# Kernel tuning notes

Hardware: AMD Instinct MI355X
Metric: run time of the kernel (lower is better)

## Reference

```python
import jax, jax.numpy as jnp
import numpy as np

EMBED_DIM = 512
NUM_HEADS = 8
HEAD_DIM = EMBED_DIM // NUM_HEADS


def setup_inputs() -> dict:
    key = jax.random.key(0)
    k_x, k_qkv, k_proj, k_pb = jax.random.split(key, 4)
    B, N, C = 2, 4096, EMBED_DIM
    x = jax.random.normal(k_x, (B, N, C), dtype=jnp.float32)
    # nn.Linear(embed_dim, 3*embed_dim, bias=False): weight [3C, C], y = x @ W.T
    s = 1.0 / np.sqrt(C)
    w_qkv = jax.random.uniform(k_qkv, (3 * C, C), dtype=jnp.float32, minval=-s, maxval=s)
    w_proj = jax.random.uniform(k_proj, (C, C), dtype=jnp.float32, minval=-s, maxval=s)
    b_proj = jax.random.uniform(k_pb, (C,), dtype=jnp.float32, minval=-s, maxval=s)
    return {"x": x, "w_qkv": w_qkv, "w_proj": w_proj, "b_proj": b_proj}


def reference(x, w_qkv, w_proj, b_proj):
    B, N, C = x.shape
    H, D = NUM_HEADS, HEAD_DIM
    scale = D ** -0.5
    qkv = jnp.einsum('bnc,fc->bnf', x, w_qkv)           # [B, N, 3C]
    qkv = qkv.reshape(B, N, 3, H, D)
    q, k, v = [jnp.transpose(qkv[:, :, i], (0, 2, 1, 3)) for i in range(3)]  # [B,H,N,D]
    attn = jnp.einsum('bhnd,bhmd->bhnm', q, k) * scale  # [B,H,N,N]
    # additive causal mask: -inf above the diagonal
    causal = jnp.triu(jnp.full((N, N), -jnp.inf, dtype=attn.dtype), k=1)
    attn = jax.nn.softmax(attn + causal, axis=-1)
    out = jnp.einsum('bhnm,bhmd->bhnd', attn, v)        # [B,H,N,D]
    out = jnp.transpose(out, (0, 2, 1, 3)).reshape(B, N, C)
    return jnp.einsum('bnc,oc->bno', out, w_proj) + b_proj
```

## Files before the change

kernel.cpp:

```cpp
#include <hip/hip_runtime.h>
#include <hip/hip_bf16.h>


typedef __attribute__((ext_vector_type(8))) short s16x8;
typedef __attribute__((ext_vector_type(4))) float f32x4;

#define QSCALE 0.18033688011112042f

__device__ __forceinline__ ushort f2bf(float f) {
  unsigned u = __float_as_uint(f);
  u = (u + 0x7FFFu + ((u >> 16) & 1u)) >> 16;
  return (ushort)u;
}

__device__ __forceinline__ unsigned cvt_pk_bf16(float a, float b) {
  unsigned r;
  asm("v_cvt_pk_bf16_f32 %0, %1, %2" : "=v"(r) : "v"(a), "v"(b));
  return r;
}

__device__ __forceinline__ float bflo(unsigned u) { return __uint_as_float(u << 16); }
__device__ __forceinline__ float bfhi(unsigned u) { return __uint_as_float(u & 0xffff0000u); }

__global__ __launch_bounds__(256) void cvt_all(const float* __restrict__ x,
                                               const float* __restrict__ wq,
                                               const float* __restrict__ wp,
                                               ushort* __restrict__ xb,
                                               ushort* __restrict__ wqb,
                                               ushort* __restrict__ wpb) {
  int i = blockIdx.x * 256 + threadIdx.x;
  const float* src;
  ushort* dst;
  int off;
  if (i < 1048576) {
    src = x; dst = xb; off = i;
  } else if (i < 1245184) {
    src = wq; dst = wqb; off = i - 1048576;
  } else {
    src = wp; dst = wpb; off = i - 1245184;
  }
  float4 v = reinterpret_cast<const float4*>(src)[off];
  ushort4 o;
  o.x = f2bf(v.x); o.y = f2bf(v.y); o.z = f2bf(v.z); o.w = f2bf(v.w);
  reinterpret_cast<ushort4*>(dst)[off] = o;
}

template <int EPI>
__global__ __launch_bounds__(256) void gemm_bt(const ushort* __restrict__ A,
                                               const ushort* __restrict__ W,
                                               ushort* __restrict__ q_ws,
                                               ushort* __restrict__ k_ws,
                                               ushort* __restrict__ vt_ws,
                                               float* __restrict__ outf,
                                               const float* __restrict__ bias) {
  __shared__ ushort As[2][128 * 32];
  __shared__ ushort Bs[2][128 * 32];
  const int tid = threadIdx.x;
  const int lane = tid & 63, wv = tid >> 6;
  const int wm = wv >> 1, wn = wv & 1;
  const int l15 = lane & 15, g = lane >> 4;
  const int tm = blockIdx.y * 128, tn = blockIdx.x * 128;

  f32x4 acc[4][4] = {};

#define GSTAGE(BUF, K0)                                                                    \
  do {                                                                                     \
    _Pragma("unroll") for (int it = 0; it < 2; ++it) {                                     \
      int slot = it * 256 + tid;                                                           \
      int row = slot >> 2;                                                                 \
      int ch = (slot & 3) ^ ((row >> 1) & 3);                                              \
      const int sb = (it * 256 + wv * 64) * 8;        \
      __builtin_amdgcn_global_load_lds(                                                    \
          (const __attribute__((address_space(1))) void*)(A + (size_t)(tm + row) * 512 +   \
                                                          (K0) + ch * 8),                  \
          (__attribute__((address_space(3))) void*)(&As[BUF][0] + sb), 16, 0, 0);          \
      __builtin_amdgcn_global_load_lds(                                                    \
          (const __attribute__((address_space(1))) void*)(W + (size_t)(tn + row) * 512 +   \
                                                          (K0) + ch * 8),                  \
          (__attribute__((address_space(3))) void*)(&Bs[BUF][0] + sb), 16, 0, 0);          \
    }                                                                                      \
  } while (0)

  GSTAGE(0, 0);
  __syncthreads();
  int cur = 0;
  for (int t = 0; t < 16; ++t) {
    if (t < 15) GSTAGE(cur ^ 1, (t + 1) * 32);
    s16x8 af[4], bfr[4];
#pragma unroll
    for (int i = 0; i < 4; ++i) {
      int Ra = wm * 64 + i * 16 + l15;
      af[i] = reinterpret_cast<const s16x8*>(&As[cur][0])[Ra * 4 + (g ^ ((Ra >> 1) & 3))];
      int Rb = wn * 64 + i * 16 + l15;
      bfr[i] = reinterpret_cast<const s16x8*>(&Bs[cur][0])[Rb * 4 + (g ^ ((Rb >> 1) & 3))];
    }
#pragma unroll
    for (int mi = 0; mi < 4; ++mi)
#pragma unroll
      for (int ni = 0; ni < 4; ++ni)
        acc[mi][ni] =
            __builtin_amdgcn_mfma_f32_16x16x32_bf16(af[mi], bfr[ni], acc[mi][ni], 0, 0, 0);
    __syncthreads();
    cur ^= 1;
  }
#undef GSTAGE

  const int rowb = tm + wm * 64 + g * 4;
  const int colb = tn + wn * 64 + l15;
#pragma unroll
  for (int mi = 0; mi < 4; ++mi) {
#pragma unroll
    for (int ni = 0; ni < 4; ++ni) {
      int r0 = rowb + mi * 16;
      int col = colb + ni * 16;
      if (EPI == 0) {
        int i3 = col >> 9, h = (col >> 6) & 7, d = col & 63;
        int b = r0 >> 12;
        int bh = b * 8 + h;
        if (i3 == 2) {
          int n0 = r0 & 4095;
          int kt = n0 >> 6, ce = (n0 >> 5) & 1, ge = (n0 >> 3) & 3, je = n0 & 7;
          int nbe = d >> 4, le = d & 15;
          ushort4 pk;
          pk.x = f2bf(acc[mi][ni][0]);
          pk.y = f2bf(acc[mi][ni][1]);
          pk.z = f2bf(acc[mi][ni][2]);
          pk.w = f2bf(acc[mi][ni][3]);
          *reinterpret_cast<ushort4*>(
              vt_ws + (((size_t)bh * 64 + kt) * 8 + nbe * 2 + ce) * 512 + (ge * 16 + le) * 8 +
              je) = pk;
        } else if (i3 == 1) {
          int ce = d >> 5, ge = (d >> 3) & 3, je = d & 7;
#pragma unroll
          for (int r = 0; r < 4; ++r) {
            int n = (r0 + r) & 4095;
            int kt = n >> 6, le = n & 15, nbe = (n >> 4) & 3;
            k_ws[(((size_t)bh * 64 + kt) * 8 + nbe * 2 + ce) * 512 + (ge * 16 + le) * 8 + je] =
                f2bf(acc[mi][ni][r]);
          }
        } else {
          int n0 = r0 & 4095;
#pragma unroll
          for (int r = 0; r < 4; ++r)
            q_ws[((size_t)bh * 4096 + (n0 + r)) * 64 + d] = f2bf(acc[mi][ni][r] * QSCALE);
        }
      } else {
#pragma unroll
        for (int r = 0; r < 4; ++r)
          outf[(size_t)(r0 + r) * 512 + col] = acc[mi][ni][r] + bias[col];
      }
    }
  }
}

__global__ __launch_bounds__(256, 3) void attn_kernel(const ushort* __restrict__ Q,
                                                      const ushort* __restrict__ Kk,
                                                      const ushort* __restrict__ Vt,
                                                      ushort* __restrict__ po,
                                                      float* __restrict__ ml) {
  __shared__ ushort Ks[2][4096];
  __shared__ ushort Vs[2][4096];
  __shared__ ushort P_lds[4][32 * 64];
  const int tid = threadIdx.x;
  const int lane = tid & 63, wv = tid >> 6;
  const int l15 = lane & 15, g = lane >> 4;
  const int L = blockIdx.x;
  const int p = L & 7;
  int j2 = L >> 3;
  {
    const int pos = j2 & 31, quarter = j2 >> 5;
    if (quarter & 1) j2 = quarter * 32 + (31 - pos);
  }
  const int bh = p * 2 + (j2 & 1);
  const int i = j2 >> 1;
  const int G = 31 - (i >> 1);
  const int h = i & 1;
  const int qt = 4 * G + wv;
  const int ktmax = qt >> 1;
  const int mid = G + 1;
  const int klo = h ? mid : 0;
  const int khi = h ? ktmax : (mid - 1);
  const int KLO = h ? mid : 0;
  const int KHI = h ? (2 * G + 1) : (mid - 1);
  const int slot = (bh * 128 + qt) * 2 + h;
  const int qw = qt * 32;
  const size_t baseQ = (size_t)bh * 4096 * 64;

  s16x8 aq[2][2];
#pragma unroll
  for (int s = 0; s < 2; ++s) {
    const ushort* qp = Q + baseQ + (size_t)(qw + s * 16 + l15) * 64 + g * 8;
    aq[s][0] = *reinterpret_cast<const s16x8*>(qp);
    aq[s][1] = *reinterpret_cast<const s16x8*>(qp + 32);
  }

  f32x4 o[2][4] = {};
  float m[2] = {-1e30f, -1e30f};
  float l[2] = {0.f, 0.f};
  const int swz = (l15 & 7) << 3;
  ushort* pl = P_lds[wv];

#define KVSTAGE(BUF, KT)                                                                  \
  do {                                                                                    \
    const ushort* kSrc = Kk + ((size_t)bh * 64 + (KT)) * 4096;                            \
    const ushort* vSrc = Vt + ((size_t)bh * 64 + (KT)) * 4096;                            \
    _Pragma("unroll") for (int c = 0; c < 2; ++c) {                                       \
      const int sb = (c * 256 + wv * 64) * 8;        \
      __builtin_amdgcn_global_load_lds(                                                   \
          (const __attribute__((address_space(1))) void*)(kSrc + sb + lane * 8),          \
          (__attribute__((address_space(3))) void*)(&Ks[BUF][0] + sb), 16, 0, 0);         \
      __builtin_amdgcn_global_load_lds(                                                   \
          (const __attribute__((address_space(1))) void*)(vSrc + sb + lane * 8),          \
          (__attribute__((address_space(3))) void*)(&Vs[BUF][0] + sb), 16, 0, 0);         \
    }                                                                                     \
  } while (0)

  KVSTAGE(0, KLO);
  __syncthreads();
  int cur = 0;
  for (int kt = KLO; kt <= KHI; ++kt) {
    if (kt < KHI) KVSTAGE(cur ^ 1, kt + 1);
    if (kt >= klo && kt <= khi) {
      const ushort* kl = &Ks[cur][lane * 8];
      const ushort* vl = &Vs[cur][lane * 8];
      s16x8 kf[8], vf[8];
#pragma unroll
      for (int t = 0; t < 8; ++t) kf[t] = *reinterpret_cast<const s16x8*>(kl + t * 512);
#pragma unroll
      for (int t = 0; t < 8; ++t) vf[t] = *reinterpret_cast<const s16x8*>(vl + t * 512);
      f32x4 st[2][4] = {};
      __builtin_amdgcn_s_setprio(1);
#pragma unroll
      for (int nb = 0; nb < 4; ++nb)
#pragma unroll
        for (int s = 0; s < 2; ++s) {
          st[s][nb] = __builtin_amdgcn_mfma_f32_16x16x32_bf16(kf[nb * 2 + 0], aq[s][0],
                                                              st[s][nb], 0, 0, 0);
          st[s][nb] = __builtin_amdgcn_mfma_f32_16x16x32_bf16(kf[nb * 2 + 1], aq[s][1],
                                                              st[s][nb], 0, 0, 0);
        }
      __builtin_amdgcn_s_setprio(0);
      if (kt == ktmax) {
        const int k0d = kt * 64;
#pragma unroll
        for (int s = 0; s < 2; ++s)
#pragma unroll
          for (int nb = 0; nb < 4; ++nb)
#pragma unroll
            for (int r2 = 0; r2 < 4; ++r2)
              if (k0d + nb * 16 + g * 4 + r2 > qw + s * 16 + l15) st[s][nb][r2] = -1e30f;
      }
#pragma unroll
      for (int s = 0; s < 2; ++s) {
        float a0 = fmaxf(fmaxf(st[s][0][0], st[s][0][1]), fmaxf(st[s][0][2], st[s][0][3]));
        float a1 = fmaxf(fmaxf(st[s][1][0], st[s][1][1]), fmaxf(st[s][1][2], st[s][1][3]));
        float a2 = fmaxf(fmaxf(st[s][2][0], st[s][2][1]), fmaxf(st[s][2][2], st[s][2][3]));
        float a3 = fmaxf(fmaxf(st[s][3][0], st[s][3][1]), fmaxf(st[s][3][2], st[s][3][3]));
        float pm = fmaxf(fmaxf(a0, a1), fmaxf(a2, a3));
        if (!__all(pm - m[s] <= 8.0f)) {
          float pmf = fmaxf(pm, __shfl_xor(pm, 16));
          pmf = fmaxf(pmf, __shfl_xor(pmf, 32));
          const float mn = fmaxf(m[s], pmf);
          const float al = __builtin_amdgcn_exp2f(m[s] - mn);
          l[s] *= al;
          m[s] = mn;
#pragma unroll
          for (int nb = 0; nb < 4; ++nb)
#pragma unroll
            for (int r2 = 0; r2 < 4; ++r2) o[s][nb][r2] *= al;
        }
        float rs = 0.f;
#pragma unroll
        for (int nb = 0; nb < 4; ++nb) {
          float p0 = __builtin_amdgcn_exp2f(st[s][nb][0] - m[s]);
          float p1 = __builtin_amdgcn_exp2f(st[s][nb][1] - m[s]);
          float p2 = __builtin_amdgcn_exp2f(st[s][nb][2] - m[s]);
          float p3 = __builtin_amdgcn_exp2f(st[s][nb][3] - m[s]);
          rs += (p0 + p1) + (p2 + p3);
          uint2 w;
          w.x = cvt_pk_bf16(p0, p1);
          w.y = cvt_pk_bf16(p2, p3);
          *reinterpret_cast<uint2*>(pl + (s * 16 + l15) * 64 + ((nb * 16 + g * 4) ^ swz)) = w;
        }
        l[s] += rs;
      }
      s16x8 pa[2][2];
#pragma unroll
      for (int s = 0; s < 2; ++s)
#pragma unroll
        for (int c = 0; c < 2; ++c)
          pa[s][c] = *reinterpret_cast<const s16x8*>(pl + (s * 16 + l15) * 64 +
                                                     ((c * 32 + g * 8) ^ swz));
      __builtin_amdgcn_s_setprio(1);
#pragma unroll
      for (int nb = 0; nb < 4; ++nb)
#pragma unroll
        for (int s = 0; s < 2; ++s) {
          o[s][nb] = __builtin_amdgcn_mfma_f32_16x16x32_bf16(vf[nb * 2 + 0], pa[s][0],
                                                             o[s][nb], 0, 0, 0);
          o[s][nb] = __builtin_amdgcn_mfma_f32_16x16x32_bf16(vf[nb * 2 + 1], pa[s][1],
                                                             o[s][nb], 0, 0, 0);
        }
      __builtin_amdgcn_s_setprio(0);
    }
    __syncthreads();
    cur ^= 1;
  }
#undef KVSTAGE

  float lr[2];
#pragma unroll
  for (int s = 0; s < 2; ++s) {
    float ls = l[s];
    ls += __shfl_xor(ls, 16);
    ls += __shfl_xor(ls, 32);
    lr[s] = ls;
  }

#pragma unroll
  for (int s = 0; s < 2; ++s) {
    const float linv = (lr[s] > 0.f) ? (1.0f / lr[s]) : 0.f;
    const int row = s * 16 + l15;
    const size_t pbase = ((size_t)slot * 32 + row) * 64;
#pragma unroll
    for (int nb = 0; nb < 4; ++nb) {
      uint2 pk;
      pk.x = cvt_pk_bf16(o[s][nb][0] * linv, o[s][nb][1] * linv);
      pk.y = cvt_pk_bf16(o[s][nb][2] * linv, o[s][nb][3] * linv);
      *reinterpret_cast<uint2*>(po + pbase + nb * 16 + g * 4) = pk;
    }
    if (g == 0) {
      float2 v;
      v.x = m[s];
      v.y = lr[s];
      *reinterpret_cast<float2*>(ml + ((size_t)slot * 32 + row) * 2) = v;
    }
  }
}

__global__ __launch_bounds__(64) void attn_merge(const ushort* __restrict__ po,
                                                 const float* __restrict__ ml,
                                                 ushort* __restrict__ O) {
  const int M = blockIdx.x, tid = threadIdx.x;
  const int p = M & 7, q2 = M >> 3;
  const int bh = p * 2 + (q2 & 1);
  const int qt = q2 >> 1;
  const int t = bh * 128 + qt;
  const int row = tid >> 1, dh = (tid & 1) * 32;
  const float2 ml0 = *reinterpret_cast<const float2*>(ml + ((size_t)(t * 2 + 0) * 32 + row) * 2);
  const float2 ml1 = *reinterpret_cast<const float2*>(ml + ((size_t)(t * 2 + 1) * 32 + row) * 2);
  const float ms = fmaxf(ml0.x, ml1.x);
  const float w0 = __builtin_amdgcn_exp2f(ml0.x - ms) * ml0.y;
  const float w1 = __builtin_amdgcn_exp2f(ml1.x - ms) * ml1.y;
  const float inv = 1.0f / (w0 + w1);
  const float c0 = w0 * inv, c1 = w1 * inv;
  const int b = bh >> 3, h = bh & 7;
  const size_t rowo = (size_t)(b * 4096 + qt * 32 + row) * 512 + h * 64 + dh;
  const ushort* p0 = po + ((size_t)(t * 2 + 0) * 32 + row) * 64 + dh;
  const ushort* p1 = po + ((size_t)(t * 2 + 1) * 32 + row) * 64 + dh;
#pragma unroll
  for (int j = 0; j < 4; ++j) {
    uint4 a = reinterpret_cast<const uint4*>(p0)[j];
    uint4 bb = reinterpret_cast<const uint4*>(p1)[j];
    uint4 out;
    out.x = cvt_pk_bf16(c0 * bflo(a.x) + c1 * bflo(bb.x), c0 * bfhi(a.x) + c1 * bfhi(bb.x));
    out.y = cvt_pk_bf16(c0 * bflo(a.y) + c1 * bflo(bb.y), c0 * bfhi(a.y) + c1 * bfhi(bb.y));
    out.z = cvt_pk_bf16(c0 * bflo(a.z) + c1 * bflo(bb.z), c0 * bfhi(a.z) + c1 * bfhi(bb.z));
    out.w = cvt_pk_bf16(c0 * bflo(a.w) + c1 * bflo(bb.w), c0 * bfhi(a.w) + c1 * bfhi(bb.w));
    reinterpret_cast<uint4*>(&O[rowo])[j] = out;
  }
}

extern "C" void kernel_launch(void* const* d_in, const int* in_sizes, int n_in,
                              void* d_out, int out_size, void* d_ws, size_t ws_size,
                              hipStream_t stream) {
  const float* x = (const float*)d_in[0];
  const float* w_qkv = (const float*)d_in[1];
  const float* w_proj = (const float*)d_in[2];
  const float* b_proj = (const float*)d_in[3];
  float* out = (float*)d_out;

  ushort* xb = (ushort*)d_ws;
  ushort* wqkvb = xb + (size_t)8192 * 512;
  ushort* wprojb = wqkvb + (size_t)1536 * 512;
  ushort* qws = wprojb + (size_t)512 * 512;
  ushort* kws = qws + (size_t)16 * 4096 * 64;
  ushort* vtws = kws + (size_t)16 * 4096 * 64;
  ushort* ows = vtws + (size_t)16 * 4096 * 64;

  cvt_all<<<5120, 256, 0, stream>>>(x, w_qkv, w_proj, xb, wqkvb, wprojb);

  gemm_bt<0><<<dim3(12, 64), 256, 0, stream>>>(xb, wqkvb, qws, kws, vtws, nullptr, nullptr);

  ushort* po = ows + (size_t)8192 * 512;
  float* ml = (float*)(po + (size_t)2048 * 2 * 32 * 64);

  attn_kernel<<<1024, 256, 0, stream>>>(qws, kws, vtws, po, ml);
  attn_merge<<<2048, 64, 0, stream>>>(po, ml, ows);

  gemm_bt<1><<<dim3(4, 64), 256, 0, stream>>>(ows, wprojb, nullptr, nullptr, nullptr, out,
                                              b_proj);
}
```

Before: 109.1 us.

## Switch attention to 32x32x16 MFMA with in-register P via permlane32 swap

Rewrites the attention inner loop to use 32x32x16 bf16 MFMA instead of 16x16x32. The Q, K and V^T workspace layouts written by the QKV GEMM epilogue are changed to match the new operand fragments. The softmax probabilities are repacked into B-operand registers with v_permlane32_swap, which removes the per-wave P LDS round trip and its extra reads and writes. Row statistics now need only a single cross-half shuffle. Occupancy hint drops from 3 to 2 blocks per CU because of larger accumulator register use, and V loads are deferred until after the softmax.

```diff
diff --git a/kernel.cpp b/kernel.cpp
--- a/kernel.cpp
+++ b/kernel.cpp
@@ -4,6 +4,8 @@
 
 typedef __attribute__((ext_vector_type(8))) short s16x8;
 typedef __attribute__((ext_vector_type(4))) float f32x4;
+typedef __attribute__((ext_vector_type(16))) float f32x16;
+typedef __attribute__((ext_vector_type(4))) unsigned u32x4;
 
 #define QSCALE 0.18033688011112042f
 
@@ -119,30 +121,35 @@
         int bh = b * 8 + h;
         if (i3 == 2) {
           int n0 = r0 & 4095;
-          int kt = n0 >> 6, ce = (n0 >> 5) & 1, ge = (n0 >> 3) & 3, je = n0 & 7;
-          int nbe = d >> 4, le = d & 15;
+          int kt64 = n0 >> 6, key64 = n0 & 63;
+          int kc = key64 >> 4, hk = (key64 >> 3) & 1, j0 = key64 & 7;
+          int db = d >> 5, d31 = d & 31;
           ushort4 pk;
           pk.x = f2bf(acc[mi][ni][0]);
           pk.y = f2bf(acc[mi][ni][1]);
           pk.z = f2bf(acc[mi][ni][2]);
           pk.w = f2bf(acc[mi][ni][3]);
-          *reinterpret_cast<ushort4*>(
-              vt_ws + (((size_t)bh * 64 + kt) * 8 + nbe * 2 + ce) * 512 + (ge * 16 + le) * 8 +
-              je) = pk;
+          *reinterpret_cast<ushort4*>(vt_ws + (size_t)(bh * 64 + kt64) * 4096 +
+                                      ((db * 4 + kc) * 64 + d31 + 32 * hk) * 8 + j0) = pk;
         } else if (i3 == 1) {
-          int ce = d >> 5, ge = (d >> 3) & 3, je = d & 7;
+          int dt = d >> 4, hd = (d >> 3) & 1, j = d & 7;
 #pragma unroll
           for (int r = 0; r < 4; ++r) {
             int n = (r0 + r) & 4095;
-            int kt = n >> 6, le = n & 15, nbe = (n >> 4) & 3;
-            k_ws[(((size_t)bh * 64 + kt) * 8 + nbe * 2 + ce) * 512 + (ge * 16 + le) * 8 + je] =
-                f2bf(acc[mi][ni][r]);
+            int kt64 = n >> 6, key64 = n & 63;
+            int kb = key64 >> 5, key31 = key64 & 31;
+            k_ws[(size_t)(bh * 64 + kt64) * 4096 +
+                 ((kb * 4 + dt) * 64 + key31 + 32 * hd) * 8 + j] = f2bf(acc[mi][ni][r]);
           }
         } else {
-          int n0 = r0 & 4095;
-#pragma unroll
-          for (int r = 0; r < 4; ++r)
-            q_ws[((size_t)bh * 4096 + (n0 + r)) * 64 + d] = f2bf(acc[mi][ni][r] * QSCALE);
+          int dt = d >> 4, hd = (d >> 3) & 1, j = d & 7;
+#pragma unroll
+          for (int r = 0; r < 4; ++r) {
+            int n = (r0 + r) & 4095;
+            int qt = n >> 5, q31 = n & 31;
+            q_ws[(size_t)(bh * 128 + qt) * 2048 + (dt * 64 + q31 + 32 * hd) * 8 + j] =
+                f2bf(acc[mi][ni][r] * QSCALE);
+          }
         }
       } else {
 #pragma unroll
@@ -153,17 +160,16 @@
   }
 }
 
-__global__ __launch_bounds__(256, 3) void attn_kernel(const ushort* __restrict__ Q,
+__global__ __launch_bounds__(256, 2) void attn_kernel(const ushort* __restrict__ Q,
                                                       const ushort* __restrict__ Kk,
                                                       const ushort* __restrict__ Vt,
                                                       ushort* __restrict__ po,
                                                       float* __restrict__ ml) {
   __shared__ ushort Ks[2][4096];
   __shared__ ushort Vs[2][4096];
-  __shared__ ushort P_lds[4][32 * 64];
   const int tid = threadIdx.x;
   const int lane = tid & 63, wv = tid >> 6;
-  const int l15 = lane & 15, g = lane >> 4;
+  const int l31 = lane & 31, hf = lane >> 5;
   const int L = blockIdx.x;
   const int p = L & 7;
   int j2 = L >> 3;
@@ -184,28 +190,24 @@
   const int KHI = h ? (2 * G + 1) : (mid - 1);
   const int slot = (bh * 128 + qt) * 2 + h;
   const int qw = qt * 32;
-  const size_t baseQ = (size_t)bh * 4096 * 64;
-
-  s16x8 aq[2][2];
-#pragma unroll
-  for (int s = 0; s < 2; ++s) {
-    const ushort* qp = Q + baseQ + (size_t)(qw + s * 16 + l15) * 64 + g * 8;
-    aq[s][0] = *reinterpret_cast<const s16x8*>(qp);
-    aq[s][1] = *reinterpret_cast<const s16x8*>(qp + 32);
-  }
-
-  f32x4 o[2][4] = {};
-  float m[2] = {-1e30f, -1e30f};
-  float l[2] = {0.f, 0.f};
-  const int swz = (l15 & 7) << 3;
-  ushort* pl = P_lds[wv];
+
+  s16x8 aq[4];
+  {
+    const ushort* qp = Q + ((size_t)bh * 128 + qt) * 2048 + lane * 8;
+#pragma unroll
+    for (int dt = 0; dt < 4; ++dt) aq[dt] = *reinterpret_cast<const s16x8*>(qp + dt * 512);
+  }
+
+  f32x16 o[2] = {};
+  float m = -1e30f;
+  float l = 0.f;
 
 #define KVSTAGE(BUF, KT)                                                                  \
   do {                                                                                    \
     const ushort* kSrc = Kk + ((size_t)bh * 64 + (KT)) * 4096;                            \
     const ushort* vSrc = Vt + ((size_t)bh * 64 + (KT)) * 4096;                            \
     _Pragma("unroll") for (int c = 0; c < 2; ++c) {                                       \
-      const int sb = (c * 256 + wv * 64) * 8;        \
+      const int sb = (c * 256 + wv * 64) * 8;                                             \
       __builtin_amdgcn_global_load_lds(                                                   \
           (const __attribute__((address_space(1))) void*)(kSrc + sb + lane * 8),          \
           (__attribute__((address_space(3))) void*)(&Ks[BUF][0] + sb), 16, 0, 0);         \
@@ -222,85 +224,85 @@
     if (kt < KHI) KVSTAGE(cur ^ 1, kt + 1);
     if (kt >= klo && kt <= khi) {
       const ushort* kl = &Ks[cur][lane * 8];
-      const ushort* vl = &Vs[cur][lane * 8];
-      s16x8 kf[8], vf[8];
+      s16x8 kf[8];
 #pragma unroll
       for (int t = 0; t < 8; ++t) kf[t] = *reinterpret_cast<const s16x8*>(kl + t * 512);
-#pragma unroll
-      for (int t = 0; t < 8; ++t) vf[t] = *reinterpret_cast<const s16x8*>(vl + t * 512);
-      f32x4 st[2][4] = {};
+      f32x16 st[2] = {};
       __builtin_amdgcn_s_setprio(1);
 #pragma unroll
-      for (int nb = 0; nb < 4; ++nb)
-#pragma unroll
-        for (int s = 0; s < 2; ++s) {
-          st[s][nb] = __builtin_amdgcn_mfma_f32_16x16x32_bf16(kf[nb * 2 + 0], aq[s][0],
-                                                              st[s][nb], 0, 0, 0);
-          st[s][nb] = __builtin_amdgcn_mfma_f32_16x16x32_bf16(kf[nb * 2 + 1], aq[s][1],
-                                                              st[s][nb], 0, 0, 0);
-        }
+      for (int kb = 0; kb < 2; ++kb)
+#pragma unroll
+        for (int dt = 0; dt < 4; ++dt)
+          st[kb] = __builtin_amdgcn_mfma_f32_32x32x16_bf16(kf[kb * 4 + dt], aq[dt],
+                                                           st[kb], 0, 0, 0);
       __builtin_amdgcn_s_setprio(0);
       if (kt == ktmax) {
-        const int k0d = kt * 64;
-#pragma unroll
-        for (int s = 0; s < 2; ++s)
-#pragma unroll
-          for (int nb = 0; nb < 4; ++nb)
-#pragma unroll
-            for (int r2 = 0; r2 < 4; ++r2)
-              if (k0d + nb * 16 + g * 4 + r2 > qw + s * 16 + l15) st[s][nb][r2] = -1e30f;
-      }
-#pragma unroll
-      for (int s = 0; s < 2; ++s) {
-        float a0 = fmaxf(fmaxf(st[s][0][0], st[s][0][1]), fmaxf(st[s][0][2], st[s][0][3]));
-        float a1 = fmaxf(fmaxf(st[s][1][0], st[s][1][1]), fmaxf(st[s][1][2], st[s][1][3]));
-        float a2 = fmaxf(fmaxf(st[s][2][0], st[s][2][1]), fmaxf(st[s][2][2], st[s][2][3]));
-        float a3 = fmaxf(fmaxf(st[s][3][0], st[s][3][1]), fmaxf(st[s][3][2], st[s][3][3]));
-        float pm = fmaxf(fmaxf(a0, a1), fmaxf(a2, a3));
-        if (!__all(pm - m[s] <= 8.0f)) {
-          float pmf = fmaxf(pm, __shfl_xor(pm, 16));
-          pmf = fmaxf(pmf, __shfl_xor(pmf, 32));
-          const float mn = fmaxf(m[s], pmf);
-          const float al = __builtin_amdgcn_exp2f(m[s] - mn);
-          l[s] *= al;
-          m[s] = mn;
-#pragma unroll
-          for (int nb = 0; nb < 4; ++nb)
-#pragma unroll
-            for (int r2 = 0; r2 < 4; ++r2) o[s][nb][r2] *= al;
+        const int qg = qw + l31;
+#pragma unroll
+        for (int kb = 0; kb < 2; ++kb)
+#pragma unroll
+          for (int r = 0; r < 16; ++r)
+            if (kt * 64 + kb * 32 + (r & 3) + 8 * (r >> 2) + 4 * hf > qg)
+              st[kb][r] = -1e30f;
+      }
+      float mx[2];
+#pragma unroll
+      for (int kb = 0; kb < 2; ++kb) {
+        float t0 = fmaxf(fmaxf(st[kb][0], st[kb][1]), fmaxf(st[kb][2], st[kb][3]));
+        float t1 = fmaxf(fmaxf(st[kb][4], st[kb][5]), fmaxf(st[kb][6], st[kb][7]));
+        float t2 = fmaxf(fmaxf(st[kb][8], st[kb][9]), fmaxf(st[kb][10], st[kb][11]));
+        float t3 = fmaxf(fmaxf(st[kb][12], st[kb][13]), fmaxf(st[kb][14], st[kb][15]));
+        mx[kb] = fmaxf(fmaxf(t0, t1), fmaxf(t2, t3));
+      }
+      float pm = fmaxf(mx[0], mx[1]);
+      if (!__all(pm - m <= 8.0f)) {
+        float pmf = fmaxf(pm, __shfl_xor(pm, 32));
+        const float mn = fmaxf(m, pmf);
+        const float al = __builtin_amdgcn_exp2f(m - mn);
+        l *= al;
+        m = mn;
+#pragma unroll
+        for (int db = 0; db < 2; ++db)
+#pragma unroll
+          for (int r = 0; r < 16; ++r) o[db][r] *= al;
+      }
+      s16x8 pb[4];
+      float rs = 0.f;
+#pragma unroll
+      for (int kb = 0; kb < 2; ++kb) {
+        float e[16];
+#pragma unroll
+        for (int r = 0; r < 16; ++r) {
+          e[r] = __builtin_amdgcn_exp2f(st[kb][r] - m);
+          rs += e[r];
         }
-        float rs = 0.f;
-#pragma unroll
-        for (int nb = 0; nb < 4; ++nb) {
-          float p0 = __builtin_amdgcn_exp2f(st[s][nb][0] - m[s]);
-          float p1 = __builtin_amdgcn_exp2f(st[s][nb][1] - m[s]);
-          float p2 = __builtin_amdgcn_exp2f(st[s][nb][2] - m[s]);
-          float p3 = __builtin_amdgcn_exp2f(st[s][nb][3] - m[s]);
-          rs += (p0 + p1) + (p2 + p3);
-          uint2 w;
-          w.x = cvt_pk_bf16(p0, p1);
-          w.y = cvt_pk_bf16(p2, p3);
-          *reinterpret_cast<uint2*>(pl + (s * 16 + l15) * 64 + ((nb * 16 + g * 4) ^ swz)) = w;
-        }
-        l[s] += rs;
-      }
-      s16x8 pa[2][2];
-#pragma unroll
-      for (int s = 0; s < 2; ++s)
-#pragma unroll
-        for (int c = 0; c < 2; ++c)
-          pa[s][c] = *reinterpret_cast<const s16x8*>(pl + (s * 16 + l15) * 64 +
-                                                     ((c * 32 + g * 8) ^ swz));
+        unsigned a0 = cvt_pk_bf16(e[0], e[1]), a1 = cvt_pk_bf16(e[2], e[3]);
+        unsigned b0 = cvt_pk_bf16(e[4], e[5]), b1 = cvt_pk_bf16(e[6], e[7]);
+        asm volatile("v_permlane32_swap_b32 %0, %1" : "+v"(a0), "+v"(b0));
+        asm volatile("v_permlane32_swap_b32 %0, %1" : "+v"(a1), "+v"(b1));
+        u32x4 w0;
+        w0[0] = a0; w0[1] = a1; w0[2] = b0; w0[3] = b1;
+        pb[kb * 2] = __builtin_bit_cast(s16x8, w0);
+        unsigned c0 = cvt_pk_bf16(e[8], e[9]), c1 = cvt_pk_bf16(e[10], e[11]);
+        unsigned d0 = cvt_pk_bf16(e[12], e[13]), d1 = cvt_pk_bf16(e[14], e[15]);
+        asm volatile("v_permlane32_swap_b32 %0, %1" : "+v"(c0), "+v"(d0));
+        asm volatile("v_permlane32_swap_b32 %0, %1" : "+v"(c1), "+v"(d1));
+        u32x4 w1;
+        w1[0] = c0; w1[1] = c1; w1[2] = d0; w1[3] = d1;
+        pb[kb * 2 + 1] = __builtin_bit_cast(s16x8, w1);
+      }
+      l += rs;
+      const ushort* vl = &Vs[cur][lane * 8];
+      s16x8 vf[8];
+#pragma unroll
+      for (int t = 0; t < 8; ++t) vf[t] = *reinterpret_cast<const s16x8*>(vl + t * 512);
       __builtin_amdgcn_s_setprio(1);
 #pragma unroll
-      for (int nb = 0; nb < 4; ++nb)
-#pragma unroll
-        for (int s = 0; s < 2; ++s) {
-          o[s][nb] = __builtin_amdgcn_mfma_f32_16x16x32_bf16(vf[nb * 2 + 0], pa[s][0],
-                                                             o[s][nb], 0, 0, 0);
-          o[s][nb] = __builtin_amdgcn_mfma_f32_16x16x32_bf16(vf[nb * 2 + 1], pa[s][1],
-                                                             o[s][nb], 0, 0, 0);
-        }
+      for (int db = 0; db < 2; ++db)
+#pragma unroll
+        for (int kc = 0; kc < 4; ++kc)
+          o[db] = __builtin_amdgcn_mfma_f32_32x32x16_bf16(vf[db * 4 + kc], pb[kc],
+                                                          o[db], 0, 0, 0);
       __builtin_amdgcn_s_setprio(0);
     }
     __syncthreads();
@@ -308,33 +310,25 @@
   }
 #undef KVSTAGE
 
-  float lr[2];
-#pragma unroll
-  for (int s = 0; s < 2; ++s) {
-    float ls = l[s];
-    ls += __shfl_xor(ls, 16);
-    ls += __shfl_xor(ls, 32);
-    lr[s] = ls;
-  }
-
-#pragma unroll
-  for (int s = 0; s < 2; ++s) {
-    const float linv = (lr[s] > 0.f) ? (1.0f / lr[s]) : 0.f;
-    const int row = s * 16 + l15;
-    const size_t pbase = ((size_t)slot * 32 + row) * 64;
-#pragma unroll
-    for (int nb = 0; nb < 4; ++nb) {
+  float lr = l + __shfl_xor(l, 32);
+  const float linv = (lr > 0.f) ? (1.0f / lr) : 0.f;
+
+  const size_t pbase = ((size_t)slot * 32 + l31) * 64;
+#pragma unroll
+  for (int db = 0; db < 2; ++db)
+#pragma unroll
+    for (int rg = 0; rg < 4; ++rg) {
+      const int d0 = db * 32 + 8 * rg + 4 * hf;
       uint2 pk;
-      pk.x = cvt_pk_bf16(o[s][nb][0] * linv, o[s][nb][1] * linv);
-      pk.y = cvt_pk_bf16(o[s][nb][2] * linv, o[s][nb][3] * linv);
-      *reinterpret_cast<uint2*>(po + pbase + nb * 16 + g * 4) = pk;
+      pk.x = cvt_pk_bf16(o[db][rg * 4 + 0] * linv, o[db][rg * 4 + 1] * linv);
+      pk.y = cvt_pk_bf16(o[db][rg * 4 + 2] * linv, o[db][rg * 4 + 3] * linv);
+      *reinterpret_cast<uint2*>(po + pbase + d0) = pk;
     }
-    if (g == 0) {
-      float2 v;
-      v.x = m[s];
-      v.y = lr[s];
-      *reinterpret_cast<float2*>(ml + ((size_t)slot * 32 + row) * 2) = v;
-    }
+  if (hf == 0) {
+    float2 v;
+    v.x = m;
+    v.y = lr;
+    *reinterpret_cast<float2*>(ml + ((size_t)slot * 32 + l31) * 2) = v;
   }
 }
 
```

Result: no change. 107.8 us (-1.1%).
